# Performance work log

Measured on AMD Instinct MI355X. Metric: run time of the kernel, lower is better.

## Reference

```python
import jax, jax.numpy as jnp
import numpy as np

D_MODEL = 1024
N_HEADS = 16
D_HEAD = D_MODEL // N_HEADS
D_FF = 2048
B, S = 4, 1024
EPS = 1e-6


def layernorm(x, gamma, beta):
    mu = jnp.mean(x, axis=-1, keepdims=True)
    var = jnp.mean(jnp.square(x - mu), axis=-1, keepdims=True)
    return (x - mu) * jax.lax.rsqrt(var + EPS) * gamma + beta


def setup_inputs() -> dict:
    key = jax.random.key(0)
    ks = jax.random.split(key, 12)
    s = 0.02
    return {
        "x": jax.random.normal(ks[0], (B, S, D_MODEL), jnp.float32),
        "mask": jnp.ones((B, 1, 1, S), jnp.int32),
        "Wq": jax.random.normal(ks[1], (D_MODEL, D_MODEL), jnp.float32) * s,
        "Wk": jax.random.normal(ks[2], (D_MODEL, D_MODEL), jnp.float32) * s,
        "Wv": jax.random.normal(ks[3], (D_MODEL, D_MODEL), jnp.float32) * s,
        "Wo": jax.random.normal(ks[4], (D_MODEL, D_MODEL), jnp.float32) * s,
        "bo": jnp.zeros((D_MODEL,), jnp.float32),
        "ln1_g": jnp.ones((D_MODEL,), jnp.float32),
        "ln1_b": jnp.zeros((D_MODEL,), jnp.float32),
        "W1": jax.random.normal(ks[5], (D_MODEL, D_FF), jnp.float32) * s,
        "b1": jnp.zeros((D_FF,), jnp.float32),
        "W2": jax.random.normal(ks[6], (D_FF, D_MODEL), jnp.float32) * s,
        "b2": jnp.zeros((D_MODEL,), jnp.float32),
        "ln2_g": jnp.ones((D_MODEL,), jnp.float32),
        "ln2_b": jnp.zeros((D_MODEL,), jnp.float32),
    }


def reference(x, mask, Wq, Wk, Wv, Wo, bo, ln1_g, ln1_b, W1, b1, W2, b2, ln2_g, ln2_b):
    b, s, _ = x.shape
    # --- multi-head attention ---
    q_proj = x @ Wq                      # [B,S,D]
    k_proj = x @ Wk
    v_proj = x @ Wv
    q = q_proj.reshape(b, s, N_HEADS, D_HEAD)
    k = k_proj.reshape(b, s, N_HEADS, D_HEAD)
    v = v_proj.reshape(b, s, N_HEADS, D_HEAD)
    attn = jnp.einsum('bqhd,bkhd->bhqk', q, k)           # [B,H,S,S]
    attn = jnp.where(mask == 0, -jnp.inf, attn)
    attn = jax.nn.softmax(attn / jnp.sqrt(jnp.float32(D_MODEL)), axis=-1)
    out = jnp.einsum('bhqk,bkhd->bqhd', attn, v).reshape(b, s, D_MODEL)
    # source applies ReLU after the output projection, dropout=eval identity
    out = jax.nn.relu(out @ Wo + bo) + q_proj            # residual = projected queries
    out = layernorm(out, ln1_g, ln1_b)
    # --- FFN (source applies activation AFTER linear2) ---
    ff = jax.nn.relu((out @ W1 + b1) @ W2 + b2) + out
    return layernorm(ff, ln2_g, ln2_b)
```

## Files before the change

kernel.cpp:

```cpp
#include <hip/hip_runtime.h>
#include <hip/hip_bf16.h>

#define D_MODEL 1024
#define N_HEADS 16
#define D_HEAD  64
#define D_FF    2048
#define BATCH   4
#define SEQ     1024
#define ROWS    (BATCH*SEQ)

typedef __bf16  bf16x8 __attribute__((ext_vector_type(8)));
typedef float   f32x4  __attribute__((ext_vector_type(4)));
typedef unsigned int u32x4 __attribute__((ext_vector_type(4)));
typedef unsigned int u32x2 __attribute__((ext_vector_type(2)));
typedef unsigned short u16;
typedef unsigned int u32;

__device__ inline u16 f2bf(float x){ __hip_bfloat16 b = __float2bfloat16(x); return *(u16*)&b; }

__device__ inline void load_lds16(const u16* gsrc, u16* ldst){
  __builtin_amdgcn_global_load_lds((const __attribute__((address_space(1))) void*)gsrc,
                                   (__attribute__((address_space(3))) void*)ldst, 16, 0, 0);
}

__global__ __launch_bounds__(256)
void cast_bf16_kernel(const float* __restrict__ src, __hip_bfloat16* __restrict__ dst, int n){
  int i = (blockIdx.x*blockDim.x + threadIdx.x)*4;
  if (i + 3 < n){
    float4 v = *(const float4*)(src + i);
    dst[i+0] = __float2bfloat16(v.x);
    dst[i+1] = __float2bfloat16(v.y);
    dst[i+2] = __float2bfloat16(v.z);
    dst[i+3] = __float2bfloat16(v.w);
  }
}

__global__ __launch_bounds__(256)
void transpose_cast_kernel(const float* __restrict__ src, __hip_bfloat16* __restrict__ dst,
                           int R, int C){
  __shared__ float tile[32][33];
  int c0 = blockIdx.x*32, r0 = blockIdx.y*32;
  int tx = threadIdx.x & 31, ty = threadIdx.x >> 5;
  #pragma unroll
  for (int i=0;i<32;i+=8)
    tile[ty+i][tx] = src[(size_t)(r0+ty+i)*C + (c0+tx)];
  __syncthreads();
  #pragma unroll
  for (int i=0;i<32;i+=8)
    dst[(size_t)(c0+ty+i)*R + (r0+tx)] = __float2bfloat16(tile[tx][ty+i]);
}

__global__ __launch_bounds__(256)
void transpose4_kernel(const float* __restrict__ s0, const float* __restrict__ s1,
                       const float* __restrict__ s2, const float* __restrict__ s3,
                       __hip_bfloat16* __restrict__ dst){
  __shared__ float tile[32][33];
  const float* src = (blockIdx.z==0)?s0:(blockIdx.z==1)?s1:(blockIdx.z==2)?s2:s3;
  __hip_bfloat16* d = dst + (size_t)blockIdx.z*1024*1024;
  int c0 = blockIdx.x*32, r0 = blockIdx.y*32;
  int tx = threadIdx.x & 31, ty = threadIdx.x >> 5;
  #pragma unroll
  for (int i=0;i<32;i+=8)
    tile[ty+i][tx] = src[(size_t)(r0+ty+i)*1024 + (c0+tx)];
  __syncthreads();
  #pragma unroll
  for (int i=0;i<32;i+=8)
    d[(size_t)(c0+ty+i)*1024 + (r0+tx)] = __float2bfloat16(tile[tx][ty+i]);
}

template<int MODE>
__global__ __launch_bounds__(256, 2)
void gemm_bt_kernel(const u16* __restrict__ A, const u16* __restrict__ BT,
                    const float* __restrict__ bias, const float* __restrict__ res,
                    float* __restrict__ Cf, __hip_bfloat16* __restrict__ Cb,
                    int M, int N, int K, float cscale){
  __shared__ u16 As[2][128*32];
  __shared__ u16 Bs[2][128*32];
  const int m0 = blockIdx.y*128, n0 = blockIdx.x*128;
  const int t = threadIdx.x;
  const int wid = t>>6, lane = t&63;
  const int wm = wid>>1, wn = wid&1;
  const int lr = lane&15, lk = (lane>>4)*8;
  const int srow = t>>2, sseg = (t&3)*8;
  const int wbase = wid*512;

  f32x4 acc[4][4] = {};

  for (int kt=0; kt<K; kt+=64){
    __syncthreads();
    #pragma unroll
    for (int half=0; half<2; ++half){
      #pragma unroll
      for (int c=0;c<2;++c){
        load_lds16(A  + (size_t)(m0 + c*64 + srow)*K + kt + half*32 + sseg, &As[half][c*2048 + wbase]);
        load_lds16(BT + (size_t)(n0 + c*64 + srow)*K + kt + half*32 + sseg, &Bs[half][c*2048 + wbase]);
      }
    }
    __syncthreads();
    #pragma unroll
    for (int half=0; half<2; ++half){
      bf16x8 af[4], bfr[4];
      #pragma unroll
      for (int f=0; f<4; ++f){
        af[f]  = *(const bf16x8*)&As[half][(wm*64 + f*16 + lr)*32 + lk];
        bfr[f] = *(const bf16x8*)&Bs[half][(wn*64 + f*16 + lr)*32 + lk];
      }
      #pragma unroll
      for (int i=0;i<4;++i)
        #pragma unroll
        for (int j=0;j<4;++j)
          acc[i][j] = __builtin_amdgcn_mfma_f32_16x16x32_bf16(af[i], bfr[j], acc[i][j], 0,0,0);
    }
  }

  const int r_in = (lane>>4)*4;
  #pragma unroll
  for (int i=0;i<4;++i){
    #pragma unroll
    for (int j=0;j<4;++j){
      int col = n0 + wn*64 + j*16 + lr;
      float bv = bias ? bias[col] : 0.f;
      #pragma unroll
      for (int e=0;e<4;++e){
        int row = m0 + wm*64 + i*16 + r_in + e;
        float v = acc[i][j][e] + bv;
        if (MODE == 0){
          Cf[(size_t)row*N + col] = v;
        } else if (MODE == 1){
          Cb[(size_t)row*N + col] = __float2bfloat16(v);
        } else if (MODE == 6){
          Cf[(size_t)row*N + col] = fmaxf(v,0.f) + res[(size_t)row*N + col];
        } else {
          int b = row>>10, s = row&1023;
          int which = col>>10, c = col&1023, h = c>>6, d = c&63;
          size_t hm = (((size_t)b*16 + h)*1024 + s)*64 + d;
          if (which == 0){
            Cf[(size_t)row*1024 + c] = v;
            Cb[hm] = __float2bfloat16(v * cscale);
          } else if (which == 1){
            Cb[4194304u + hm] = __float2bfloat16(v);
          } else {
            Cb[8388608u + (((size_t)b*16 + h)*64 + d)*1024 + s] = __float2bfloat16(v);
          }
        }
      }
    }
  }
}

__global__ __launch_bounds__(512)
void attn_mfma_kernel(const u16* __restrict__ qb, const u16* __restrict__ kb,
                      const u16* __restrict__ vt, const int* __restrict__ mask,
                      __hip_bfloat16* __restrict__ out){
  __shared__ u16 Ks[2][64*72];
  __shared__ u16 Vs[2][64*72];
  __shared__ u16 Pl[8][16*72];
  const int t = threadIdx.x;
  const int wid = t>>6, lane = t&63;
  const int lr = lane&15, lg = lane>>4, lk = lg*8;
  const int bid = blockIdx.x;
  const int xcd = bid & 7, slot = bid >> 3;
  const int bh = xcd*8 + (slot>>3);
  const int qx = slot & 7;
  const int b = bh>>4, h = bh&15;
  const int q0 = qx*128 + wid*16;
  const u16* qbase = qb + (size_t)bh*1024*64;
  const u16* kbase = kb + (size_t)bh*1024*64;
  const u16* vbase = vt + (size_t)bh*64*1024;
  const int* mrow = mask + b*SEQ;

  bf16x8 aq[2];
  aq[0] = *(const bf16x8*)(qbase + (size_t)(q0+lr)*64 + lk);
  aq[1] = *(const bf16x8*)(qbase + (size_t)(q0+lr)*64 + 32 + lk);

  f32x4 osum[4] = {};
  float m1 = -1e30f, l1 = 0.f;

  const int sr = t>>3, sg = (t&7)*8;
  {
    u32x4 kr = *(const u32x4*)(kbase + (size_t)sr*64 + sg);
    u32x4 vr = *(const u32x4*)(vbase + (size_t)sr*1024 + sg);
    *(u32x4*)&Ks[0][sr*72+sg] = kr;
    *(u32x4*)&Vs[0][sr*72+sg] = vr;
  }
  __syncthreads();

  for (int kt=0; kt<SEQ/64; ++kt){
    const int k0 = kt*64;
    const int cur = kt&1;
    u32x4 kr, vr;
    const bool more = (kt+1 < SEQ/64);
    if (more){
      kr = *(const u32x4*)(kbase + (size_t)(k0+64+sr)*64 + sg);
      vr = *(const u32x4*)(vbase + (size_t)sr*1024 + (k0+64) + sg);
    }

    unsigned long long bm = __ballot(mrow[k0 + lane] != 0);

    f32x4 sacc[4] = {};
    __builtin_amdgcn_s_setprio(1);
    #pragma unroll
    for (int k4=0;k4<4;++k4){
      #pragma unroll
      for (int dg=0;dg<2;++dg){
        bf16x8 kf = *(const bf16x8*)&Ks[cur][(k4*16+lr)*72 + dg*32 + lk];
        sacc[k4] = __builtin_amdgcn_mfma_f32_16x16x32_bf16(kf, aq[dg], sacc[k4],0,0,0);
      }
    }
    __builtin_amdgcn_s_setprio(0);
    if (bm != ~0ull){
      #pragma unroll
      for (int k4=0;k4<4;++k4)
        #pragma unroll
        for (int e=0;e<4;++e)
          if (!((bm >> (k4*16 + lg*4 + e)) & 1)) sacc[k4][e] = -1e30f;
    }

    float tm = -1e30f;
    #pragma unroll
    for (int k4=0;k4<4;++k4)
      #pragma unroll
      for (int e=0;e<4;++e) tm = fmaxf(tm, sacc[k4][e]);
    tm = fmaxf(tm, __shfl_xor(tm,16));
    tm = fmaxf(tm, __shfl_xor(tm,32));

    float mn = m1, c = 1.f;
    bool need = !__all(tm <= m1 + 8.f);
    if (need){
      mn = fmaxf(m1, tm);
      c  = exp2f(m1 - mn);
      m1 = mn;
    }
    float ps = 0.f;
    #pragma unroll
    for (int k4=0;k4<4;++k4)
      #pragma unroll
      for (int e=0;e<4;++e){ float p = exp2f(sacc[k4][e]-mn); sacc[k4][e]=p; ps+=p; }
    ps += __shfl_xor(ps,16);
    ps += __shfl_xor(ps,32);
    l1 = l1*c + ps;

    if (need){
      float ce[4];
      #pragma unroll
      for (int e=0;e<4;++e) ce[e] = __shfl(c, lg*4+e);
      #pragma unroll
      for (int dt=0;dt<4;++dt)
        #pragma unroll
        for (int e=0;e<4;++e) osum[dt][e] *= ce[e];
    }

    #pragma unroll
    for (int k4=0;k4<4;++k4){
      u32 lo = (u32)f2bf(sacc[k4][0]) | ((u32)f2bf(sacc[k4][1])<<16);
      u32 hi = (u32)f2bf(sacc[k4][2]) | ((u32)f2bf(sacc[k4][3])<<16);
      u32x2 pk; pk[0]=lo; pk[1]=hi;
      *(u32x2*)&Pl[wid][lr*72 + k4*16 + lg*4] = pk;
    }
    __builtin_amdgcn_s_setprio(1);
    #pragma unroll
    for (int dt=0;dt<4;++dt){
      #pragma unroll
      for (int kg=0;kg<2;++kg){
        bf16x8 pa = *(const bf16x8*)&Pl[wid][lr*72 + kg*32 + lk];
        bf16x8 vf = *(const bf16x8*)&Vs[cur][(dt*16+lr)*72 + kg*32 + lk];
        osum[dt] = __builtin_amdgcn_mfma_f32_16x16x32_bf16(pa, vf, osum[dt],0,0,0);
      }
    }
    __builtin_amdgcn_s_setprio(0);

    if (more){
      *(u32x4*)&Ks[cur^1][sr*72+sg] = kr;
      *(u32x4*)&Vs[cur^1][sr*72+sg] = vr;
    }
    __syncthreads();
  }
  float li[4];
  #pragma unroll
  for (int e=0;e<4;++e) li[e] = 1.f / __shfl(l1, lg*4+e);
  #pragma unroll
  for (int dt=0;dt<4;++dt){
    int d = dt*16 + lr;
    #pragma unroll
    for (int e=0;e<4;++e){
      int q = q0 + lg*4 + e;
      out[((size_t)b*1024 + q)*1024 + h*64 + d] = __float2bfloat16(osum[dt][e] * li[e]);
    }
  }
}

__global__ __launch_bounds__(256)
void ln_kernel(const float* __restrict__ a, const float* __restrict__ g,
               const float* __restrict__ be, float* __restrict__ outf,
               __hip_bfloat16* __restrict__ outb){
  int row = blockIdx.x, t = threadIdx.x;
  size_t rb = (size_t)row*D_MODEL;
  float4 av = *(const float4*)(a + rb + t*4);
  float v0 = av.x, v1 = av.y, v2 = av.z, v3 = av.w;
  float sum = v0+v1+v2+v3;
  float ss  = v0*v0+v1*v1+v2*v2+v3*v3;
  #pragma unroll
  for (int off=32; off; off>>=1){ sum += __shfl_xor(sum,off); ss += __shfl_xor(ss,off); }
  __shared__ float red[8];
  int wid = t>>6, lane = t&63;
  if (lane==0){ red[wid]=sum; red[4+wid]=ss; }
  __syncthreads();
  sum = red[0]+red[1]+red[2]+red[3];
  ss  = red[4]+red[5]+red[6]+red[7];
  float mu  = sum*(1.f/1024.f);
  float var = ss*(1.f/1024.f) - mu*mu;
  float rstd = rsqrtf(var + 1e-6f);
  float4 gv = *(const float4*)(g  + t*4);
  float4 bv = *(const float4*)(be + t*4);
  float y0=(v0-mu)*rstd*gv.x+bv.x;
  float y1=(v1-mu)*rstd*gv.y+bv.y;
  float y2=(v2-mu)*rstd*gv.z+bv.z;
  float y3=(v3-mu)*rstd*gv.w+bv.w;
  *(float4*)(outf+rb+t*4) = make_float4(y0,y1,y2,y3);
  if (outb){
    outb[rb+t*4+0]=__float2bfloat16(y0);
    outb[rb+t*4+1]=__float2bfloat16(y1);
    outb[rb+t*4+2]=__float2bfloat16(y2);
    outb[rb+t*4+3]=__float2bfloat16(y3);
  }
}

extern "C" void kernel_launch(void* const* d_in, const int* in_sizes, int n_in,
                              void* d_out, int out_size, void* d_ws, size_t ws_size,
                              hipStream_t stream){
  const float* x    = (const float*)d_in[0];
  const int*   mask = (const int*)  d_in[1];
  const float* Wq   = (const float*)d_in[2];
  const float* Wk   = (const float*)d_in[3];
  const float* Wv   = (const float*)d_in[4];
  const float* Wo   = (const float*)d_in[5];
  const float* bo   = (const float*)d_in[6];
  const float* ln1g = (const float*)d_in[7];
  const float* ln1b = (const float*)d_in[8];
  const float* W1   = (const float*)d_in[9];
  const float* b1   = (const float*)d_in[10];
  const float* W2   = (const float*)d_in[11];
  const float* b2   = (const float*)d_in[12];
  const float* ln2g = (const float*)d_in[13];
  const float* ln2b = (const float*)d_in[14];

  char* ws = (char*)d_ws;
  const size_t MB = 1024*1024;
  __hip_bfloat16* WqT  = (__hip_bfloat16*)(ws + 0);
  __hip_bfloat16* WoT  = (__hip_bfloat16*)(ws + 6*MB);
  __hip_bfloat16* W1T  = (__hip_bfloat16*)(ws + 8*MB);
  __hip_bfloat16* W2T  = (__hip_bfloat16*)(ws + 12*MB);
  __hip_bfloat16* xb   = (__hip_bfloat16*)(ws + 16*MB);
  float* q_proj        = (float*)(ws + 24*MB);
  __hip_bfloat16* qb   = (__hip_bfloat16*)(ws + 40*MB);
  __hip_bfloat16* attn_o = (__hip_bfloat16*)(ws + 64*MB);
  float* t1f           = (float*)(ws + 40*MB);
  float* h1f           = (float*)(ws + 56*MB);
  __hip_bfloat16* h1b  = (__hip_bfloat16*)(ws + 16*MB);
  __hip_bfloat16* ff1b = (__hip_bfloat16*)(ws + 24*MB);
  float* t2f           = (float*)(ws + 40*MB);

  const float qscale = 0.03125f * 1.44269504f;

  cast_bf16_kernel<<<ROWS*D_MODEL/4/256, 256, 0, stream>>>(x, xb, ROWS*D_MODEL);
  transpose4_kernel<<<dim3(32,32,4), 256, 0, stream>>>(Wq, Wk, Wv, Wo, WqT);
  transpose_cast_kernel<<<dim3(64,32), 256, 0, stream>>>(W1, W1T, 1024, 2048);
  transpose_cast_kernel<<<dim3(32,64), 256, 0, stream>>>(W2, W2T, 2048, 1024);

  gemm_bt_kernel<5><<<dim3(24,32), 256, 0, stream>>>((const u16*)xb, (const u16*)WqT, nullptr,
                                                     nullptr, q_proj, qb, ROWS, 3072, 1024, qscale);

  attn_mfma_kernel<<<512, 512, 0, stream>>>(
      (const u16*)qb, (const u16*)(qb + 4194304u), (const u16*)(qb + 8388608u), mask, attn_o);

  gemm_bt_kernel<6><<<dim3(8,32), 256, 0, stream>>>((const u16*)attn_o, (const u16*)WoT, bo,
                                                    q_proj, t1f, nullptr, ROWS, 1024, 1024, 1.f);

  ln_kernel<<<ROWS, 256, 0, stream>>>(t1f, ln1g, ln1b, h1f, h1b);

  gemm_bt_kernel<1><<<dim3(16,32), 256, 0, stream>>>((const u16*)h1b, (const u16*)W1T, b1,
                                                     nullptr, nullptr, ff1b, ROWS, 2048, 1024, 1.f);

  gemm_bt_kernel<6><<<dim3(8,32), 256, 0, stream>>>((const u16*)ff1b, (const u16*)W2T, b2,
                                                    h1f, t2f, nullptr, ROWS, 1024, 2048, 1.f);

  ln_kernel<<<ROWS, 256, 0, stream>>>(t2f, ln2g, ln2b, (float*)d_out, nullptr);
}
```

Baseline: 209.1 us.

## Double-buffer GEMM LDS tiles and use narrower N tiles for N=1024 GEMMs

The bf16 MFMA GEMM now keeps two LDS stages. It prefetches the next K-slab with global_load_lds while the current slab feeds the MFMAs, and drops to one barrier per iteration. This is meant to hide global-memory latency that the old load/sync/compute loop exposed. The kernel also takes the N tile width as a template parameter, and the two N=1024 GEMMs (Wo and W2) use 64-wide tiles so they launch twice as many blocks and fill more CUs. The cost is doubled LDS per block, which for the 128-wide variant may limit occupancy, and lower per-block reuse in the narrow-tile case.

```diff
diff --git a/kernel.cpp b/kernel.cpp
--- a/kernel.cpp
+++ b/kernel.cpp
@@ -68,15 +68,15 @@
     d[(size_t)(c0+ty+i)*1024 + (r0+tx)] = __float2bfloat16(tile[tx][ty+i]);
 }
 
-template<int MODE>
+template<int MODE, int BN>
 __global__ __launch_bounds__(256, 2)
 void gemm_bt_kernel(const u16* __restrict__ A, const u16* __restrict__ BT,
                     const float* __restrict__ bias, const float* __restrict__ res,
                     float* __restrict__ Cf, __hip_bfloat16* __restrict__ Cb,
                     int M, int N, int K, float cscale){
-  __shared__ u16 As[2][128*32];
-  __shared__ u16 Bs[2][128*32];
-  const int m0 = blockIdx.y*128, n0 = blockIdx.x*128;
+  __shared__ u16 As[2][2][128*32];
+  __shared__ u16 Bs[2][2][BN*32];
+  const int m0 = blockIdx.y*128, n0 = blockIdx.x*BN;
   const int t = threadIdx.x;
   const int wid = t>>6, lane = t&63;
   const int wm = wid>>1, wn = wid&1;
@@ -84,41 +84,61 @@
   const int srow = t>>2, sseg = (t&3)*8;
   const int wbase = wid*512;
 
-  f32x4 acc[4][4] = {};
-
-  for (int kt=0; kt<K; kt+=64){
-    __syncthreads();
+  constexpr int NJ = BN/32;
+  f32x4 acc[4][NJ] = {};
+  const int NK = K/64;
+
+  #pragma unroll
+  for (int half=0; half<2; ++half){
+    #pragma unroll
+    for (int c=0;c<2;++c)
+      load_lds16(A + (size_t)(m0 + c*64 + srow)*K + half*32 + sseg, &As[0][half][c*2048 + wbase]);
+    #pragma unroll
+    for (int c=0;c<BN/64;++c)
+      load_lds16(BT + (size_t)(n0 + c*64 + srow)*K + half*32 + sseg, &Bs[0][half][c*2048 + wbase]);
+  }
+  __syncthreads();
+
+  for (int kt=0; kt<NK; ++kt){
+    const int cur = kt&1;
+    if (kt+1 < NK){
+      const int kn = (kt+1)*64;
+      #pragma unroll
+      for (int half=0; half<2; ++half){
+        #pragma unroll
+        for (int c=0;c<2;++c)
+          load_lds16(A + (size_t)(m0 + c*64 + srow)*K + kn + half*32 + sseg,
+                     &As[cur^1][half][c*2048 + wbase]);
+        #pragma unroll
+        for (int c=0;c<BN/64;++c)
+          load_lds16(BT + (size_t)(n0 + c*64 + srow)*K + kn + half*32 + sseg,
+                     &Bs[cur^1][half][c*2048 + wbase]);
+      }
+    }
     #pragma unroll
     for (int half=0; half<2; ++half){
-      #pragma unroll
-      for (int c=0;c<2;++c){
-        load_lds16(A  + (size_t)(m0 + c*64 + srow)*K + kt + half*32 + sseg, &As[half][c*2048 + wbase]);
-        load_lds16(BT + (size_t)(n0 + c*64 + srow)*K + kt + half*32 + sseg, &Bs[half][c*2048 + wbase]);
-      }
-    }
-    __syncthreads();
-    #pragma unroll
-    for (int half=0; half<2; ++half){
-      bf16x8 af[4], bfr[4];
-      #pragma unroll
-      for (int f=0; f<4; ++f){
-        af[f]  = *(const bf16x8*)&As[half][(wm*64 + f*16 + lr)*32 + lk];
-        bfr[f] = *(const bf16x8*)&Bs[half][(wn*64 + f*16 + lr)*32 + lk];
-      }
+      bf16x8 af[4], bfr[NJ];
+      #pragma unroll
+      for (int f=0; f<4; ++f)
+        af[f]  = *(const bf16x8*)&As[cur][half][(wm*64 + f*16 + lr)*32 + lk];
+      #pragma unroll
+      for (int j=0; j<NJ; ++j)
+        bfr[j] = *(const bf16x8*)&Bs[cur][half][(wn*(BN/2) + j*16 + lr)*32 + lk];
       #pragma unroll
       for (int i=0;i<4;++i)
         #pragma unroll
-        for (int j=0;j<4;++j)
+        for (int j=0;j<NJ;++j)
           acc[i][j] = __builtin_amdgcn_mfma_f32_16x16x32_bf16(af[i], bfr[j], acc[i][j], 0,0,0);
     }
+    __syncthreads();
   }
 
   const int r_in = (lane>>4)*4;
   #pragma unroll
   for (int i=0;i<4;++i){
     #pragma unroll
-    for (int j=0;j<4;++j){
-      int col = n0 + wn*64 + j*16 + lr;
+    for (int j=0;j<NJ;++j){
+      int col = n0 + wn*(BN/2) + j*16 + lr;
       float bv = bias ? bias[col] : 0.f;
       #pragma unroll
       for (int e=0;e<4;++e){
@@ -367,21 +387,21 @@
   transpose_cast_kernel<<<dim3(64,32), 256, 0, stream>>>(W1, W1T, 1024, 2048);
   transpose_cast_kernel<<<dim3(32,64), 256, 0, stream>>>(W2, W2T, 2048, 1024);
 
-  gemm_bt_kernel<5><<<dim3(24,32), 256, 0, stream>>>((const u16*)xb, (const u16*)WqT, nullptr,
+  gemm_bt_kernel<5,128><<<dim3(24,32), 256, 0, stream>>>((const u16*)xb, (const u16*)WqT, nullptr,
                                                      nullptr, q_proj, qb, ROWS, 3072, 1024, qscale);
 
   attn_mfma_kernel<<<512, 512, 0, stream>>>(
       (const u16*)qb, (const u16*)(qb + 4194304u), (const u16*)(qb + 8388608u), mask, attn_o);
 
-  gemm_bt_kernel<6><<<dim3(8,32), 256, 0, stream>>>((const u16*)attn_o, (const u16*)WoT, bo,
+  gemm_bt_kernel<6,64><<<dim3(16,32), 256, 0, stream>>>((const u16*)attn_o, (const u16*)WoT, bo,
                                                     q_proj, t1f, nullptr, ROWS, 1024, 1024, 1.f);
 
   ln_kernel<<<ROWS, 256, 0, stream>>>(t1f, ln1g, ln1b, h1f, h1b);
 
-  gemm_bt_kernel<1><<<dim3(16,32), 256, 0, stream>>>((const u16*)h1b, (const u16*)W1T, b1,
+  gemm_bt_kernel<1,128><<<dim3(16,32), 256, 0, stream>>>((const u16*)h1b, (const u16*)W1T, b1,
                                                      nullptr, nullptr, ff1b, ROWS, 2048, 1024, 1.f);
 
-  gemm_bt_kernel<6><<<dim3(8,32), 256, 0, stream>>>((const u16*)ff1b, (const u16*)W2T, b2,
+  gemm_bt_kernel<6,64><<<dim3(16,32), 256, 0, stream>>>((const u16*)ff1b, (const u16*)W2T, b2,
                                                     h1f, t2f, nullptr, ROWS, 1024, 2048, 1.f);
 
   ln_kernel<<<ROWS, 256, 0, stream>>>(t2f, ln2g, ln2b, (float*)d_out, nullptr);
```

Result: no change. 212.3 us (+1.5%).
